# Performance work log

Measured on AMD Instinct MI355X. Metric: run time of the kernel, lower is better.

Reference implementation:

```python
import jax, jax.numpy as jnp
import numpy as np

N = 32768   # total nodes
E = 524288  # total edges (avg degree 16)
D = 128     # dim_h == input_size
H = 4       # attention heads
B = 64      # graphs per batch
S = 512     # nodes per graph (N = B*S, equal-size graphs)
EPS = 1e-5


def _lin(key, out_d, in_d):
    kw, kb = jax.random.split(key)
    s = 1.0 / np.sqrt(in_d)
    W = jax.random.uniform(kw, (out_d, in_d), minval=-s, maxval=s, dtype=jnp.float32)
    b = jax.random.uniform(kb, (out_d,), minval=-s, maxval=s, dtype=jnp.float32)
    return W, b


def setup_inputs() -> dict:
    key = jax.random.key(0)
    ks = jax.random.split(key, 16)
    x = jax.random.normal(ks[0], (N, D), dtype=jnp.float32)
    edge_index = jax.random.randint(ks[1], (2, E), 0, N, dtype=jnp.int64)
    batch_ids = (jnp.arange(N) // S).astype(jnp.int64)
    Wres, bres = _lin(ks[2], D, D)          # res_lin (MLPStack([in, dim_h]))
    Wk, bk = _lin(ks[3], D, D)              # ResGatedGraphConv lin_key
    Wq, bq = _lin(ks[4], D, D)              # lin_query
    Wv, bv = _lin(ks[5], D, D)              # lin_value
    Wskip, bskip = _lin(ks[6], D, D)        # lin_skip
    in_proj_w, in_proj_b = _lin(ks[7], 3 * D, D)   # MHA in_proj
    out_proj_w, out_proj_b = _lin(ks[8], D, D)     # MHA out_proj
    W1, b1 = _lin(ks[9], 2 * D, D)          # ff_linear1
    W2, b2 = _lin(ks[10], D, 2 * D)         # ff_linear2
    g1l = jax.random.normal(ks[11], (D,), dtype=jnp.float32) * 0.1 + 1.0
    b1l = jax.random.normal(ks[12], (D,), dtype=jnp.float32) * 0.1
    g1a = jax.random.normal(ks[13], (D,), dtype=jnp.float32) * 0.1 + 1.0
    b1a = jax.random.normal(ks[14], (D,), dtype=jnp.float32) * 0.1
    kg, kb2 = jax.random.split(ks[15])
    g2 = jax.random.normal(kg, (D,), dtype=jnp.float32) * 0.1 + 1.0
    b2g = jax.random.normal(kb2, (D,), dtype=jnp.float32) * 0.1
    return dict(x=x, edge_index=edge_index, batch_ids=batch_ids,
                Wres=Wres, bres=bres, Wk=Wk, bk=bk, Wq=Wq, bq=bq, Wv=Wv, bv=bv,
                Wskip=Wskip, bskip=bskip, g1l=g1l, b1l=b1l, g1a=g1a, b1a=b1a,
                in_proj_w=in_proj_w, in_proj_b=in_proj_b,
                out_proj_w=out_proj_w, out_proj_b=out_proj_b,
                W1=W1, b1=b1, W2=W2, b2=b2, g2=g2, b2g=b2g)


def _bn(h, g, b):
    # BatchNorm1d in eval mode, running_mean=0, running_var=1
    return h * (g / jnp.sqrt(1.0 + EPS)) + b


def _forward(x, edge_index, Wres, bres, Wk, bk, Wq, bq, Wv, bv, Wskip, bskip,
             g1l, b1l, g1a, b1a, in_proj_w, in_proj_b, out_proj_w, out_proj_b,
             W1, b1, W2, b2, g2, b2g):
    src, dst = edge_index[0], edge_index[1]
    # residual projection (MLPStack([input_size, dim_h]) -> Linear + ReLU)
    h_in1 = jax.nn.relu(x @ Wres.T + bres)

    # --- local: ResGatedGraphConv ---
    k = x @ Wk.T + bk   # keyed by target node
    q = x @ Wq.T + bq   # queried by source node
    v = x @ Wv.T + bv
    msg = jax.nn.sigmoid(k[dst] + q[src]) * v[src]                 # [E, D]
    agg = jax.ops.segment_sum(msg, dst, num_segments=N)            # [N, D]
    h_local = agg + (x @ Wskip.T + bskip)
    h_local = _bn(h_in1 + h_local, g1l, b1l)

    # --- global: dense-batch multihead attention (equal graphs, no padding) ---
    hd = D // H
    h_dense = h_in1.reshape(B, S, D)
    qkv = h_dense @ in_proj_w.T + in_proj_b                        # [B, S, 3D]
    qh, kh, vh = jnp.split(qkv, 3, axis=-1)
    qh = qh.reshape(B, S, H, hd)
    kh = kh.reshape(B, S, H, hd)
    vh = vh.reshape(B, S, H, hd)
    scores = jnp.einsum('bqhd,bkhd->bhqk', qh, kh) / np.sqrt(hd)   # [B, H, S, S]
    attn = jax.nn.softmax(scores, axis=-1)
    ctx = jnp.einsum('bhqk,bkhd->bqhd', attn, vh).reshape(B, S, D)
    h_attn = (ctx @ out_proj_w.T + out_proj_b).reshape(N, D)
    h_attn = _bn(h_in1 + h_attn, g1a, b1a)

    # --- combine + FFN ---
    h = h_local + h_attn
    ff = jax.nn.relu(h @ W1.T + b1) @ W2.T + b2
    h = _bn(h + ff, g2, b2g)
    return h


def reference(x, edge_index, batch_ids, Wres, bres, Wk, bk, Wq, bq, Wv, bv,
              Wskip, bskip, g1l, b1l, g1a, b1a, in_proj_w, in_proj_b,
              out_proj_w, out_proj_b, W1, b1, W2, b2, g2, b2g):
    return _forward(x, edge_index, Wres, bres, Wk, bk, Wq, bq, Wv, bv,
                    Wskip, bskip, g1l, b1l, g1a, b1a, in_proj_w, in_proj_b,
                    out_proj_w, out_proj_b, W1, b1, W2, b2, g2, b2g)
```

## Files before the change

### kernel.cpp

```cpp
#include <hip/hip_runtime.h>
#include <math.h>

#define N_NODES 32768
#define N_EDGES 524288
#define DIM     128
#define CAP     80

static constexpr size_t NM = (size_t)N_NODES * DIM;

typedef __attribute__((ext_vector_type(8)))  short bf8;
typedef __attribute__((ext_vector_type(4)))  float f32x4;
typedef __attribute__((ext_vector_type(16))) float f32x16;

__device__ __forceinline__ short f2bs(float x) {
    union { float f; unsigned int u; } v; v.f = x;
    unsigned int r = v.u + 0x7fffu + ((v.u >> 16) & 1u);
    return (short)(r >> 16);
}
__device__ __forceinline__ unsigned int pk2(float a, float b) {
    return (unsigned int)(unsigned short)f2bs(a) |
           ((unsigned int)(unsigned short)f2bs(b) << 16);
}
__device__ __forceinline__ float2 bs2f(unsigned int u) {
    union { unsigned int a; float f; } lo, hi;
    lo.a = u << 16; hi.a = u & 0xffff0000u;
    float2 r; r.x = lo.f; r.y = hi.f; return r;
}
__device__ __forceinline__ float bs1f(short s) {
    union { unsigned int a; float f; } t;
    t.a = ((unsigned int)(unsigned short)s) << 16; return t.f;
}

__global__ __launch_bounds__(256)
void cvt_scatter_kernel(const float* __restrict__ x,
                        const float* __restrict__ w0, const float* __restrict__ w1,
                        const float* __restrict__ w2, const float* __restrict__ w3,
                        const float* __restrict__ w4, const float* __restrict__ w5,
                        const float* __restrict__ w6, const float* __restrict__ w7,
                        const float* __restrict__ w8,
                        const float* __restrict__ b0, const float* __restrict__ b1,
                        const float* __restrict__ b2, const float* __restrict__ b3,
                        const float* __restrict__ b4,
                        const int* __restrict__ ei,
                        short* __restrict__ xb, short* __restrict__ wbf,
                        float* __restrict__ bcat,
                        int* __restrict__ deg, unsigned short* __restrict__ slots)
{
    if (blockIdx.x < 2048) {
        int e = blockIdx.x * 256 + threadIdx.x;
        int d = ei[N_EDGES + e];
        int pos = atomicAdd(&deg[d], 1);
        if (pos < CAP) slots[d * CAP + pos] = (unsigned short)ei[e];
        return;
    }
    long long t = (long long)(blockIdx.x - 2048) * 256 + threadIdx.x;
    long long i4 = t * 4;
    if (i4 < (long long)NM) {
        float4 v = *(const float4*)(x + i4);
        short4 o; o.x = f2bs(v.x); o.y = f2bs(v.y); o.z = f2bs(v.z); o.w = f2bs(v.w);
        *(short4*)(xb + i4) = o;
    } else {
        int j = (int)(i4 - (long long)NM);
        if (j < 212992) {
            const float* src; int off;
            if      (j <  16384) { src = w0; off = 0; }
            else if (j <  32768) { src = w1; off = 16384; }
            else if (j <  49152) { src = w2; off = 32768; }
            else if (j <  65536) { src = w3; off = 49152; }
            else if (j <  81920) { src = w4; off = 65536; }
            else if (j < 131072) { src = w5; off = 81920; }
            else if (j < 147456) { src = w6; off = 131072; }
            else if (j < 180224) { src = w7; off = 147456; }
            else                 { src = w8; off = 180224; }
            float4 v = *(const float4*)(src + (j - off));
            short4 o; o.x = f2bs(v.x); o.y = f2bs(v.y); o.z = f2bs(v.z); o.w = f2bs(v.w);
            *(short4*)(wbf + j) = o;
        } else if (j < 213632) {
            int jb = j - 212992;
            int grp = jb >> 7, loc = jb & 127;
            const float* bs = (grp == 0) ? b0 : (grp == 1) ? b1 :
                              (grp == 2) ? b2 : (grp == 3) ? b3 : b4;
            float4 v = *(const float4*)(bs + loc);
            *(float4*)(bcat + jb) = v;
        }
    }
}

__global__ __launch_bounds__(256)
void proj5_kernel(const short* __restrict__ xb, const short* __restrict__ wbf,
                  const float* __restrict__ bcat,
                  short* __restrict__ hin1b, short* __restrict__ kbv,
                  short* __restrict__ qvb, short* __restrict__ skipb)
{
    const int g  = blockIdx.x / 512;
    const int my = blockIdx.x % 512;
    const int lane = threadIdx.x & 63;
    const int wid  = threadIdx.x >> 6;
    const int m0 = my * 64 + (wid >> 1) * 32;
    const int n0 = (wid & 1) * 64;
    const int lrow = lane & 15;
    const int lk   = (lane >> 4) * 8;

    f32x4 acc[2][4] = {};
    const short* Ap = xb + (size_t)(m0 + lrow) * 128 + lk;
    const short* Wp = wbf + g * 16384 + (size_t)(n0 + lrow) * 128 + lk;
    #pragma unroll
    for (int ks = 0; ks < 128; ks += 32) {
        bf8 af[2], wf[4];
        af[0] = *(const bf8*)(Ap + ks);
        af[1] = *(const bf8*)(Ap + 16 * 128 + ks);
        #pragma unroll
        for (int j = 0; j < 4; ++j) wf[j] = *(const bf8*)(Wp + (size_t)j * 16 * 128 + ks);
        #pragma unroll
        for (int i = 0; i < 2; ++i)
            #pragma unroll
            for (int j = 0; j < 4; ++j)
                acc[i][j] = __builtin_amdgcn_mfma_f32_16x16x32_bf16(af[i], wf[j], acc[i][j], 0, 0, 0);
    }
    const int rbase = (lane >> 4) * 4;
    #pragma unroll
    for (int j = 0; j < 4; ++j) {
        int col = n0 + j * 16 + lrow;
        float bcol = bcat[g * 128 + col];
        #pragma unroll
        for (int i = 0; i < 2; ++i)
            #pragma unroll
            for (int r = 0; r < 4; ++r) {
                int row = m0 + i * 16 + rbase + r;
                float v = acc[i][j][r] + bcol;
                if (g == 0)      { v = fmaxf(v, 0.f); hin1b[(size_t)row * 128 + col] = f2bs(v); }
                else if (g == 1) kbv[(size_t)row * 128 + col] = f2bs(v);
                else if (g == 2) qvb[(size_t)row * 256 + col * 2] = f2bs(v);
                else if (g == 3) qvb[(size_t)row * 256 + col * 2 + 1] = f2bs(v);
                else             skipb[(size_t)row * 128 + col] = f2bs(v);
            }
    }
}

__global__ __launch_bounds__(256)
void inproj_kernel(const short* __restrict__ hin1b, const short* __restrict__ wbf,
                   const float* __restrict__ bin, short* __restrict__ qkvb,
                   float qscale)
{
    const int gx = blockIdx.x % 3;
    const int my = blockIdx.x / 3;
    const int lane = threadIdx.x & 63;
    const int wid  = threadIdx.x >> 6;
    const int m0 = my * 64 + (wid >> 1) * 32;
    const int n0 = (wid & 1) * 64;
    const int lrow = lane & 15;
    const int lk   = (lane >> 4) * 8;

    f32x4 acc[2][4] = {};
    const short* Ap = hin1b + (size_t)(m0 + lrow) * 128 + lk;
    const short* Wp = wbf + 81920 + (size_t)(gx * 128 + n0 + lrow) * 128 + lk;
    #pragma unroll
    for (int ks = 0; ks < 128; ks += 32) {
        bf8 af[2], wf[4];
        af[0] = *(const bf8*)(Ap + ks);
        af[1] = *(const bf8*)(Ap + 16 * 128 + ks);
        #pragma unroll
        for (int j = 0; j < 4; ++j) wf[j] = *(const bf8*)(Wp + (size_t)j * 16 * 128 + ks);
        #pragma unroll
        for (int i = 0; i < 2; ++i)
            #pragma unroll
            for (int j = 0; j < 4; ++j)
                acc[i][j] = __builtin_amdgcn_mfma_f32_16x16x32_bf16(af[i], wf[j], acc[i][j], 0, 0, 0);
    }
    const int rbase = (lane >> 4) * 4;
    #pragma unroll
    for (int j = 0; j < 4; ++j) {
        int col = gx * 128 + n0 + j * 16 + lrow;
        float bcol = bin[col];
        float sc = (col < 128) ? qscale : 1.0f;
        #pragma unroll
        for (int i = 0; i < 2; ++i)
            #pragma unroll
            for (int r = 0; r < 4; ++r) {
                int row = m0 + i * 16 + rbase + r;
                float v = (acc[i][j][r] + bcol) * sc;
                qkvb[(size_t)row * 384 + col] = f2bs(v);
            }
    }
}

__global__ __launch_bounds__(256)
void gather_local_kernel(const unsigned int* __restrict__ kbu,
                         const uint2* __restrict__ qvu,
                         const unsigned int* __restrict__ skipu,
                         const unsigned int* __restrict__ hin1u,
                         const int* __restrict__ deg,
                         const unsigned short* __restrict__ slots,
                         const float* __restrict__ g, const float* __restrict__ beta,
                         unsigned int* __restrict__ hlocal_u)
{
    const int d    = blockIdx.x * 4 + (threadIdx.x >> 6);
    const int lane = threadIdx.x & 63;
    const float rs = 0.9999950000374998f;

    float2 k2 = bs2f(kbu[(size_t)d * 64 + lane]);
    int dg = deg[d]; if (dg > CAP) dg = CAP;
    const unsigned short* sp = slots + (size_t)d * CAP;
    int i = 0;

    float ax = 0.f, ay = 0.f, cx = 0.f, cy = 0.f;
    for (; i + 8 <= dg; i += 8) {
        int s[8];
        #pragma unroll
        for (int u = 0; u < 8; ++u) s[u] = sp[i + u];
        uint2 w[8];
        #pragma unroll
        for (int u = 0; u < 8; ++u) w[u] = qvu[(size_t)s[u] * 64 + lane];
        #pragma unroll
        for (int u = 0; u < 8; ++u) {
            float2 pa = bs2f(w[u].x), pb = bs2f(w[u].y);
            if (u & 1) {
                cx += pa.y * __builtin_amdgcn_rcpf(1.0f + __expf(-(k2.x + pa.x)));
                cy += pb.y * __builtin_amdgcn_rcpf(1.0f + __expf(-(k2.y + pb.x)));
            } else {
                ax += pa.y * __builtin_amdgcn_rcpf(1.0f + __expf(-(k2.x + pa.x)));
                ay += pb.y * __builtin_amdgcn_rcpf(1.0f + __expf(-(k2.y + pb.x)));
            }
        }
    }
    for (; i + 4 <= dg; i += 4) {
        int s0 = sp[i], s1 = sp[i + 1], s2 = sp[i + 2], s3 = sp[i + 3];
        uint2 w0 = qvu[(size_t)s0 * 64 + lane];
        uint2 w1 = qvu[(size_t)s1 * 64 + lane];
        uint2 w2 = qvu[(size_t)s2 * 64 + lane];
        uint2 w3 = qvu[(size_t)s3 * 64 + lane];
        float2 p0 = bs2f(w0.x), p1 = bs2f(w0.y);
        float2 p2 = bs2f(w1.x), p3 = bs2f(w1.y);
        float2 p4 = bs2f(w2.x), p5 = bs2f(w2.y);
        float2 p6 = bs2f(w3.x), p7 = bs2f(w3.y);
        ax += p0.y * __builtin_amdgcn_rcpf(1.0f + __expf(-(k2.x + p0.x)));
        ay += p1.y * __builtin_amdgcn_rcpf(1.0f + __expf(-(k2.y + p1.x)));
        cx += p2.y * __builtin_amdgcn_rcpf(1.0f + __expf(-(k2.x + p2.x)));
        cy += p3.y * __builtin_amdgcn_rcpf(1.0f + __expf(-(k2.y + p3.x)));
        ax += p4.y * __builtin_amdgcn_rcpf(1.0f + __expf(-(k2.x + p4.x)));
        ay += p5.y * __builtin_amdgcn_rcpf(1.0f + __expf(-(k2.y + p5.x)));
        cx += p6.y * __builtin_amdgcn_rcpf(1.0f + __expf(-(k2.x + p6.x)));
        cy += p7.y * __builtin_amdgcn_rcpf(1.0f + __expf(-(k2.y + p7.x)));
    }
    for (; i < dg; ++i) {
        int s0 = sp[i];
        uint2 w0 = qvu[(size_t)s0 * 64 + lane];
        float2 p0 = bs2f(w0.x), p1 = bs2f(w0.y);
        ax += p0.y * __builtin_amdgcn_rcpf(1.0f + __expf(-(k2.x + p0.x)));
        ay += p1.y * __builtin_amdgcn_rcpf(1.0f + __expf(-(k2.y + p1.x)));
    }
    ax += cx; ay += cy;

    float2 sk = bs2f(skipu[(size_t)d * 64 + lane]);
    float2 hi = bs2f(hin1u[(size_t)d * 64 + lane]);
    float2 gv = *(const float2*)(g + lane * 2);
    float2 bt = *(const float2*)(beta + lane * 2);
    float ox = (hi.x + sk.x + ax) * (gv.x * rs) + bt.x;
    float oy = (hi.y + sk.y + ay) * (gv.y * rs) + bt.y;
    hlocal_u[(size_t)d * 64 + lane] = pk2(ox, oy);
}

__device__ __forceinline__ void lswap(unsigned int& X, unsigned int& Y, bool hi) {
    unsigned int Xs = (unsigned int)__shfl_xor((int)X, 32);
    unsigned int Ys = (unsigned int)__shfl_xor((int)Y, 32);
    unsigned int Xn = hi ? Ys : X;
    unsigned int Yn = hi ? Y  : Xs;
    X = Xn; Y = Yn;
}

__global__ __launch_bounds__(512)
void attn_mfma(const short* __restrict__ qkv, short* __restrict__ ctx)
{
    __shared__ __align__(16) char lds[36864];

    const int blk  = blockIdx.x;
    const int h    = blk & 3;
    const int b    = blk >> 2;
    const int tid  = threadIdx.x;
    const int lane = tid & 63;
    const int wid  = tid >> 6;
    const int lq = lane & 31;
    const int lg = lane >> 5;
    const size_t gbase = (size_t)(b * 512) * 384 + h * 32;

    const int skey  = tid >> 2;
    const int spart = tid & 3;
    const int vp    = tid & 63;
    const int vdq   = tid >> 6;

    bf8    kst;
    short4 v0s, v1s;

    #define STAGE_LOAD(ck)                                                     \
        kst = *(const bf8*)(qkv + gbase +                                      \
                (size_t)((ck) * 128 + skey) * 384 + 128 + spart * 8);          \
        {                                                                      \
            const short* vr = qkv + gbase +                                    \
                (size_t)((ck) * 128 + 2 * vp) * 384 + 256 + vdq * 4;           \
            v0s = *(const short4*)(vr);                                        \
            v1s = *(const short4*)(vr + 384);                                  \
        }

    #define STAGE_WRITE(s)                                                     \
        *(bf8*)((short*)(lds + (s) * 10240) + skey * 40 + spart * 8) = kst;    \
        {                                                                      \
            char* vb = lds + 20480 + (s) * 8192;                               \
            short v0a[4] = {v0s.x, v0s.y, v0s.z, v0s.w};                       \
            short v1a[4] = {v1s.x, v1s.y, v1s.z, v1s.w};                       \
            _Pragma("unroll")                                                  \
            for (int j = 0; j < 4; ++j) {                                      \
                int d = vdq * 4 + j;                                           \
                unsigned int w = (unsigned int)(unsigned short)v0a[j] |        \
                                 ((unsigned int)(unsigned short)v1a[j] << 16); \
                *(unsigned int*)(vb + d * 256 + ((4 * vp) ^ ((d & 7) << 4))) = w; \
            }                                                                  \
        }

    const int qoff = wid * 64;
    bf8 qf[2][2];
    #pragma unroll
    for (int qg = 0; qg < 2; ++qg)
        #pragma unroll
        for (int kh = 0; kh < 2; ++kh)
            qf[qg][kh] = *(const bf8*)(qkv + gbase +
                           (size_t)(qoff + qg * 32 + lq) * 384 + kh * 16 + lg * 8);

    const f32x16 Z16 = {0.f,0.f,0.f,0.f,0.f,0.f,0.f,0.f,0.f,0.f,0.f,0.f,0.f,0.f,0.f,0.f};
    f32x16 o[2] = {Z16, Z16};
    float mreg[2] = {-1e30f, -1e30f};
    float lreg[2] = {0.f, 0.f};
    const bool hiw = (lg != 0);

    STAGE_LOAD(0);
    STAGE_WRITE(0);
    __syncthreads();

    for (int c = 0; c < 4; ++c) {
        if (c < 3) { STAGE_LOAD(c + 1); }
        const short* Kb = (const short*)(lds + (c & 1) * 10240);
        const char*  Vb = lds + 20480 + (c & 1) * 8192;

        #pragma unroll
        for (int ktl = 0; ktl < 4; ++ktl) {
            bf8 ak[2], vt[2];
            #pragma unroll
            for (int kh = 0; kh < 2; ++kh) {
                ak[kh] = *(const bf8*)(Kb + (ktl * 32 + lq) * 40 + kh * 16 + lg * 8);
                int kbyte = (ktl * 32 + kh * 16 + lg * 8) * 2;
                vt[kh] = *(const bf8*)(Vb + lq * 256 + (kbyte ^ ((lq & 7) << 4)));
            }
            #pragma unroll
            for (int qg = 0; qg < 2; ++qg) {
                f32x16 s = Z16;
                s = __builtin_amdgcn_mfma_f32_32x32x16_bf16(ak[0], qf[qg][0], s, 0, 0, 0);
                s = __builtin_amdgcn_mfma_f32_32x32x16_bf16(ak[1], qf[qg][1], s, 0, 0, 0);
                float t0 = fmaxf(fmaxf(s[0],  s[1]),  s[2]);
                float t1 = fmaxf(fmaxf(s[3],  s[4]),  s[5]);
                float t2 = fmaxf(fmaxf(s[6],  s[7]),  s[8]);
                float t3 = fmaxf(fmaxf(s[9],  s[10]), s[11]);
                float t4 = fmaxf(fmaxf(s[12], s[13]), s[14]);
                float mt = fmaxf(fmaxf(fmaxf(t0, t1), t2), fmaxf(fmaxf(t3, t4), s[15]));
                mt = fmaxf(mt, __shfl_xor(mt, 32));
                if (__any(mt > mreg[qg] + 11.5415603f)) {
                    float mnew = fmaxf(mreg[qg], mt);
                    float corr = exp2f(mreg[qg] - mnew);
                    mreg[qg] = mnew;
                    lreg[qg] *= corr;
                    #pragma unroll
                    for (int r = 0; r < 16; ++r) o[qg][r] *= corr;
                }
                float m = mreg[qg];
                float p[16]; float ps = 0.f;
                #pragma unroll
                for (int r = 0; r < 16; ++r) { p[r] = exp2f(s[r] - m); ps += p[r]; }
                ps += __shfl_xor(ps, 32);
                lreg[qg] += ps;
                unsigned int w0 = pk2(p[0],  p[1]),  w1 = pk2(p[2],  p[3]);
                unsigned int w2 = pk2(p[4],  p[5]),  w3 = pk2(p[6],  p[7]);
                unsigned int w4 = pk2(p[8],  p[9]),  w5 = pk2(p[10], p[11]);
                unsigned int w6 = pk2(p[12], p[13]), w7 = pk2(p[14], p[15]);
                lswap(w0, w2, hiw); lswap(w1, w3, hiw);
                lswap(w4, w6, hiw); lswap(w5, w7, hiw);
                union { unsigned int u[4]; bf8 v; } P0, P1;
                P0.u[0] = w0; P0.u[1] = w1; P0.u[2] = w2; P0.u[3] = w3;
                P1.u[0] = w4; P1.u[1] = w5; P1.u[2] = w6; P1.u[3] = w7;
                o[qg] = __builtin_amdgcn_mfma_f32_32x32x16_bf16(vt[0], P0.v, o[qg], 0, 0, 0);
                o[qg] = __builtin_amdgcn_mfma_f32_32x32x16_bf16(vt[1], P1.v, o[qg], 0, 0, 0);
            }
        }
        if (c < 3) { STAGE_WRITE((c + 1) & 1); }
        __syncthreads();
    }
    #undef STAGE_LOAD
    #undef STAGE_WRITE

    #pragma unroll
    for (int qg = 0; qg < 2; ++qg) {
        float inv = 1.0f / lreg[qg];
        int ql = qoff + qg * 32 + lq;
        #pragma unroll
        for (int b4 = 0; b4 < 4; ++b4) {
            short4 pkv;
            pkv.x = f2bs(o[qg][b4 * 4 + 0] * inv);
            pkv.y = f2bs(o[qg][b4 * 4 + 1] * inv);
            pkv.z = f2bs(o[qg][b4 * 4 + 2] * inv);
            pkv.w = f2bs(o[qg][b4 * 4 + 3] * inv);
            int dbyte = (8 * b4 + 4 * lg) * 2;
            *(short4*)(lds + ql * 64 + (dbyte ^ ((ql & 7) << 3))) = pkv;
        }
    }
    __syncthreads();
    {
        int ql = tid;
        short* dst = ctx + (size_t)(b * 512 + ql) * 128 + h * 32;
        #pragma unroll
        for (int i = 0; i < 8; ++i) {
            short4 part = *(short4*)(lds + ql * 64 + ((i * 8) ^ ((ql & 7) << 3)));
            *(short4*)(dst + i * 4) = part;
        }
    }
}

__global__ __launch_bounds__(256)
void outproj_ff_kernel(const short* __restrict__ ctxb, const short* __restrict__ wbf,
                       const float* __restrict__ bout,
                       const short* __restrict__ hin1b, const short* __restrict__ hlocb,
                       const float* __restrict__ g1a, const float* __restrict__ b1a,
                       const float* __restrict__ b1, const float* __restrict__ b2,
                       const float* __restrict__ g2, const float* __restrict__ b2g,
                       float* __restrict__ out)
{
    __shared__ __align__(16) short ldsH[64 * 128];
    __shared__ __align__(16) short ldsF[64 * 256];
    const int my = blockIdx.x;
    const int lane = threadIdx.x & 63;
    const int wid  = threadIdx.x >> 6;
    const int lrow = lane & 15;
    const int lk   = (lane >> 4) * 8;
    const int rbase = (lane >> 4) * 4;
    const float rs = 0.9999950000374998f;

    {
        const int m0 = (wid >> 1) * 32;
        const int n0 = (wid & 1) * 64;
        f32x4 acc[2][4] = {};
        const short* Ap = ctxb + (size_t)(my * 64 + m0 + lrow) * 128 + lk;
        const short* Wp = wbf + 131072 + (size_t)(n0 + lrow) * 128 + lk;
        #pragma unroll
        for (int ks = 0; ks < 128; ks += 32) {
            bf8 af[2], wf[4];
            af[0] = *(const bf8*)(Ap + ks);
            af[1] = *(const bf8*)(Ap + 16 * 128 + ks);
            #pragma unroll
            for (int j = 0; j < 4; ++j) wf[j] = *(const bf8*)(Wp + (size_t)j * 16 * 128 + ks);
            #pragma unroll
            for (int i = 0; i < 2; ++i)
                #pragma unroll
                for (int j = 0; j < 4; ++j)
                    acc[i][j] = __builtin_amdgcn_mfma_f32_16x16x32_bf16(af[i], wf[j], acc[i][j], 0, 0, 0);
        }
        #pragma unroll
        for (int j = 0; j < 4; ++j) {
            int col = n0 + j * 16 + lrow;
            float bcol = bout[col];
            float gsc = g1a[col] * rs;
            float bsc = b1a[col];
            #pragma unroll
            for (int i = 0; i < 2; ++i)
                #pragma unroll
                for (int r = 0; r < 4; ++r) {
                    int rl = m0 + i * 16 + rbase + r;
                    size_t idx = (size_t)(my * 64 + rl) * 128 + col;
                    float v = acc[i][j][r] + bcol;
                    float o = bs1f(hlocb[idx]) + (bs1f(hin1b[idx]) + v) * gsc + bsc;
                    int byte = (rl * 256 + col * 2) ^ ((rl & 7) << 4);
                    *(short*)((char*)ldsH + byte) = f2bs(o);
                }
        }
    }
    __syncthreads();
    {
        const int m0 = (wid >> 1) * 32;
        const int n0 = (wid & 1) * 128;
        f32x4 acc[2][8] = {};
        const short* Wp = wbf + 147456 + (size_t)(n0 + lrow) * 128 + lk;
        #pragma unroll
        for (int ks = 0; ks < 128; ks += 32) {
            bf8 af[2], wf[8];
            #pragma unroll
            for (int i = 0; i < 2; ++i) {
                int row = m0 + lrow + i * 16;
                int byte = (row * 256 + (ks + lk) * 2) ^ ((row & 7) << 4);
                af[i] = *(const bf8*)((const char*)ldsH + byte);
            }
            #pragma unroll
            for (int j = 0; j < 8; ++j) wf[j] = *(const bf8*)(Wp + (size_t)j * 16 * 128 + ks);
            #pragma unroll
            for (int i = 0; i < 2; ++i)
                #pragma unroll
                for (int j = 0; j < 8; ++j)
                    acc[i][j] = __builtin_amdgcn_mfma_f32_16x16x32_bf16(af[i], wf[j], acc[i][j], 0, 0, 0);
        }
        #pragma unroll
        for (int j = 0; j < 8; ++j) {
            int col = n0 + j * 16 + lrow;
            float bc = b1[col];
            #pragma unroll
            for (int i = 0; i < 2; ++i)
                #pragma unroll
                for (int r = 0; r < 4; ++r) {
                    int rl = m0 + i * 16 + rbase + r;
                    float v = fmaxf(acc[i][j][r] + bc, 0.f);
                    int byte = (rl * 512 + col * 2) ^ ((rl & 7) << 4);
                    *(short*)((char*)ldsF + byte) = f2bs(v);
                }
        }
    }
    __syncthreads();
    {
        const int m0 = (wid >> 1) * 32;
        const int n0 = (wid & 1) * 64;
        f32x4 acc[2][4] = {};
        const short* Wp = wbf + 180224 + (size_t)(n0 + lrow) * 256 + lk;
        #pragma unroll
        for (int ks = 0; ks < 256; ks += 32) {
            bf8 af[2], wf[4];
            #pragma unroll
            for (int i = 0; i < 2; ++i) {
                int row = m0 + lrow + i * 16;
                int byte = (row * 512 + (ks + lk) * 2) ^ ((row & 7) << 4);
                af[i] = *(const bf8*)((const char*)ldsF + byte);
            }
            #pragma unroll
            for (int j = 0; j < 4; ++j) wf[j] = *(const bf8*)(Wp + (size_t)j * 16 * 256 + ks);
            #pragma unroll
            for (int i = 0; i < 2; ++i)
                #pragma unroll
                for (int j = 0; j < 4; ++j)
                    acc[i][j] = __builtin_amdgcn_mfma_f32_16x16x32_bf16(af[i], wf[j], acc[i][j], 0, 0, 0);
        }
        #pragma unroll
        for (int j = 0; j < 4; ++j) {
            int col = n0 + j * 16 + lrow;
            float bc = b2[col];
            float gsc = g2[col] * rs;
            float bsc = b2g[col];
            #pragma unroll
            for (int i = 0; i < 2; ++i)
                #pragma unroll
                for (int r = 0; r < 4; ++r) {
                    int rl = m0 + i * 16 + rbase + r;
                    int hbyte = (rl * 256 + col * 2) ^ ((rl & 7) << 4);
                    float hres = bs1f(*(const short*)((const char*)ldsH + hbyte));
                    float v = acc[i][j][r] + bc;
                    out[(size_t)(my * 64 + rl) * 128 + col] = (hres + v) * gsc + bsc;
                }
        }
    }
}

extern "C" void kernel_launch(void* const* d_in, const int* in_sizes, int n_in,
                              void* d_out, int out_size, void* d_ws, size_t ws_size,
                              hipStream_t stream)
{
    (void)in_sizes; (void)n_in; (void)out_size; (void)ws_size;

    const float* x    = (const float*)d_in[0];
    const int*   ei   = (const int*)d_in[1];
    const float* Wres = (const float*)d_in[3];
    const float* bres = (const float*)d_in[4];
    const float* Wk   = (const float*)d_in[5];
    const float* bk   = (const float*)d_in[6];
    const float* Wq   = (const float*)d_in[7];
    const float* bq   = (const float*)d_in[8];
    const float* Wv   = (const float*)d_in[9];
    const float* bv   = (const float*)d_in[10];
    const float* Wsk  = (const float*)d_in[11];
    const float* bsk  = (const float*)d_in[12];
    const float* g1l  = (const float*)d_in[13];
    const float* b1l  = (const float*)d_in[14];
    const float* g1a  = (const float*)d_in[15];
    const float* b1a  = (const float*)d_in[16];
    const float* Win  = (const float*)d_in[17];
    const float* bin  = (const float*)d_in[18];
    const float* Wout = (const float*)d_in[19];
    const float* bout = (const float*)d_in[20];
    const float* W1   = (const float*)d_in[21];
    const float* b1   = (const float*)d_in[22];
    const float* W2   = (const float*)d_in[23];
    const float* b2   = (const float*)d_in[24];
    const float* g2   = (const float*)d_in[25];
    const float* b2g  = (const float*)d_in[26];
    float* out = (float*)d_out;

    float* ws = (float*)d_ws;
    short* hin1b = (short*)ws;
    short* kbv   = (short*)(ws + NM / 2);
    short* qvb   = (short*)(ws + NM);
    short* skipb = (short*)(ws + 2 * NM);
    short* xb    = (short*)(ws + 2 * NM + NM / 2);
    short* qkvb  = (short*)(ws + 3 * NM);
    short* hlocb = (short*)(ws + 4 * NM + NM / 2);
    int* deg = (int*)(ws + 5 * NM);
    unsigned short* slots = (unsigned short*)(deg + N_NODES);
    short* ctxb  = (short*)(ws + 5 * NM);
    short* wbf   = (short*)(ws + 6 * NM);
    float* bcat  = ws + 6 * NM + 106496;

    dim3 blk(256);
    const float qscale = 0.17677669529663687f * 1.4426950408889634f;

    hipMemsetAsync((void*)deg, 0, N_NODES * sizeof(int), stream);

    cvt_scatter_kernel<<<dim3(6353), blk, 0, stream>>>(
        x, Wres, Wk, Wq, Wv, Wsk, Win, Wout, W1, W2,
        bres, bk, bq, bv, bsk, ei, xb, wbf, bcat, deg, slots);

    proj5_kernel<<<dim3(2560), blk, 0, stream>>>(
        xb, wbf, bcat, hin1b, kbv, qvb, skipb);

    inproj_kernel<<<dim3(1536), blk, 0, stream>>>(
        hin1b, wbf, bin, qkvb, qscale);

    gather_local_kernel<<<dim3(N_NODES / 4), blk, 0, stream>>>(
        (const unsigned int*)kbv, (const uint2*)qvb, (const unsigned int*)skipb,
        (const unsigned int*)hin1b, deg, slots, g1l, b1l,
        (unsigned int*)hlocb);

    attn_mfma<<<dim3(256), dim3(512), 0, stream>>>(qkvb, ctxb);

    outproj_ff_kernel<<<dim3(512), blk, 0, stream>>>(
        ctxb, wbf, bout, hin1b, hlocb, g1a, b1a, b1, b2, g2, b2g, out);
}
```

Measured before the change: 205.7 us.

## Split attention query rows across two blocks per head and truncate P to bf16

The attention kernel now launches twice as many blocks. Each block covers half of a graph's queries for one head, and each wave handles 32 query rows instead of 64. On a chip with 256 CUs, 256 blocks means about one block per CU, so this raises occupancy and cuts per-thread register pressure. The cost is that K/V staging is repeated in both blocks. The softmax probabilities are also packed to bf16 by truncation instead of round-to-nearest, which saves ALU work but adds a small bias.

```diff
diff --git a/kernel.cpp b/kernel.cpp
--- a/kernel.cpp
+++ b/kernel.cpp
@@ -20,6 +20,10 @@
 __device__ __forceinline__ unsigned int pk2(float a, float b) {
     return (unsigned int)(unsigned short)f2bs(a) |
            ((unsigned int)(unsigned short)f2bs(b) << 16);
+}
+__device__ __forceinline__ unsigned int pk2t(float a, float b) {
+    union { float f; unsigned int u; } ua, ub; ua.f = a; ub.f = b;
+    return (ua.u >> 16) | (ub.u & 0xffff0000u);
 }
 __device__ __forceinline__ float2 bs2f(unsigned int u) {
     union { unsigned int a; float f; } lo, hi;
@@ -274,8 +278,9 @@
     __shared__ __align__(16) char lds[36864];
 
     const int blk  = blockIdx.x;
-    const int h    = blk & 3;
-    const int b    = blk >> 2;
+    const int half = blk & 1;
+    const int h    = (blk >> 1) & 3;
+    const int b    = blk >> 3;
     const int tid  = threadIdx.x;
     const int lane = tid & 63;
     const int wid  = tid >> 6;
@@ -316,19 +321,17 @@
             }                                                                  \
         }
 
-    const int qoff = wid * 64;
-    bf8 qf[2][2];
+    const int qoff = half * 256 + wid * 32;
+    bf8 qf[2];
     #pragma unroll
-    for (int qg = 0; qg < 2; ++qg)
-        #pragma unroll
-        for (int kh = 0; kh < 2; ++kh)
-            qf[qg][kh] = *(const bf8*)(qkv + gbase +
-                           (size_t)(qoff + qg * 32 + lq) * 384 + kh * 16 + lg * 8);
+    for (int kh = 0; kh < 2; ++kh)
+        qf[kh] = *(const bf8*)(qkv + gbase +
+                       (size_t)(qoff + lq) * 384 + kh * 16 + lg * 8);
 
     const f32x16 Z16 = {0.f,0.f,0.f,0.f,0.f,0.f,0.f,0.f,0.f,0.f,0.f,0.f,0.f,0.f,0.f,0.f};
-    f32x16 o[2] = {Z16, Z16};
-    float mreg[2] = {-1e30f, -1e30f};
-    float lreg[2] = {0.f, 0.f};
+    f32x16 o = Z16;
+    float mreg = -1e30f;
+    float lreg = 0.f;
     const bool hiw = (lg != 0);
 
     STAGE_LOAD(0);
@@ -349,44 +352,41 @@
                 int kbyte = (ktl * 32 + kh * 16 + lg * 8) * 2;
                 vt[kh] = *(const bf8*)(Vb + lq * 256 + (kbyte ^ ((lq & 7) << 4)));
             }
-            #pragma unroll
-            for (int qg = 0; qg < 2; ++qg) {
-                f32x16 s = Z16;
-                s = __builtin_amdgcn_mfma_f32_32x32x16_bf16(ak[0], qf[qg][0], s, 0, 0, 0);
-                s = __builtin_amdgcn_mfma_f32_32x32x16_bf16(ak[1], qf[qg][1], s, 0, 0, 0);
-                float t0 = fmaxf(fmaxf(s[0],  s[1]),  s[2]);
-                float t1 = fmaxf(fmaxf(s[3],  s[4]),  s[5]);
-                float t2 = fmaxf(fmaxf(s[6],  s[7]),  s[8]);
-                float t3 = fmaxf(fmaxf(s[9],  s[10]), s[11]);
-                float t4 = fmaxf(fmaxf(s[12], s[13]), s[14]);
-                float mt = fmaxf(fmaxf(fmaxf(t0, t1), t2), fmaxf(fmaxf(t3, t4), s[15]));
-                mt = fmaxf(mt, __shfl_xor(mt, 32));
-                if (__any(mt > mreg[qg] + 11.5415603f)) {
-                    float mnew = fmaxf(mreg[qg], mt);
-                    float corr = exp2f(mreg[qg] - mnew);
-                    mreg[qg] = mnew;
-                    lreg[qg] *= corr;
-                    #pragma unroll
-                    for (int r = 0; r < 16; ++r) o[qg][r] *= corr;
-                }
-                float m = mreg[qg];
-                float p[16]; float ps = 0.f;
+            f32x16 s = Z16;
+            s = __builtin_amdgcn_mfma_f32_32x32x16_bf16(ak[0], qf[0], s, 0, 0, 0);
+            s = __builtin_amdgcn_mfma_f32_32x32x16_bf16(ak[1], qf[1], s, 0, 0, 0);
+            float t0 = fmaxf(fmaxf(s[0],  s[1]),  s[2]);
+            float t1 = fmaxf(fmaxf(s[3],  s[4]),  s[5]);
+            float t2 = fmaxf(fmaxf(s[6],  s[7]),  s[8]);
+            float t3 = fmaxf(fmaxf(s[9],  s[10]), s[11]);
+            float t4 = fmaxf(fmaxf(s[12], s[13]), s[14]);
+            float mt = fmaxf(fmaxf(fmaxf(t0, t1), t2), fmaxf(fmaxf(t3, t4), s[15]));
+            mt = fmaxf(mt, __shfl_xor(mt, 32));
+            if (__any(mt > mreg + 11.5415603f)) {
+                float mnew = fmaxf(mreg, mt);
+                float corr = exp2f(mreg - mnew);
+                mreg = mnew;
+                lreg *= corr;
                 #pragma unroll
-                for (int r = 0; r < 16; ++r) { p[r] = exp2f(s[r] - m); ps += p[r]; }
-                ps += __shfl_xor(ps, 32);
-                lreg[qg] += ps;
-                unsigned int w0 = pk2(p[0],  p[1]),  w1 = pk2(p[2],  p[3]);
-                unsigned int w2 = pk2(p[4],  p[5]),  w3 = pk2(p[6],  p[7]);
-                unsigned int w4 = pk2(p[8],  p[9]),  w5 = pk2(p[10], p[11]);
-                unsigned int w6 = pk2(p[12], p[13]), w7 = pk2(p[14], p[15]);
-                lswap(w0, w2, hiw); lswap(w1, w3, hiw);
-                lswap(w4, w6, hiw); lswap(w5, w7, hiw);
-                union { unsigned int u[4]; bf8 v; } P0, P1;
-                P0.u[0] = w0; P0.u[1] = w1; P0.u[2] = w2; P0.u[3] = w3;
-                P1.u[0] = w4; P1.u[1] = w5; P1.u[2] = w6; P1.u[3] = w7;
-                o[qg] = __builtin_amdgcn_mfma_f32_32x32x16_bf16(vt[0], P0.v, o[qg], 0, 0, 0);
-                o[qg] = __builtin_amdgcn_mfma_f32_32x32x16_bf16(vt[1], P1.v, o[qg], 0, 0, 0);
+                for (int r = 0; r < 16; ++r) o[r] *= corr;
             }
+            float m = mreg;
+            float p[16]; float ps = 0.f;
+            #pragma unroll
+            for (int r = 0; r < 16; ++r) { p[r] = exp2f(s[r] - m); ps += p[r]; }
+            ps += __shfl_xor(ps, 32);
+            lreg += ps;
+            unsigned int w0 = pk2t(p[0],  p[1]),  w1 = pk2t(p[2],  p[3]);
+            unsigned int w2 = pk2t(p[4],  p[5]),  w3 = pk2t(p[6],  p[7]);
+            unsigned int w4 = pk2t(p[8],  p[9]),  w5 = pk2t(p[10], p[11]);
+            unsigned int w6 = pk2t(p[12], p[13]), w7 = pk2t(p[14], p[15]);
+            lswap(w0, w2, hiw); lswap(w1, w3, hiw);
+            lswap(w4, w6, hiw); lswap(w5, w7, hiw);
+            union { unsigned int u[4]; bf8 v; } P0, P1;
+            P0.u[0] = w0; P0.u[1] = w1; P0.u[2] = w2; P0.u[3] = w3;
+            P1.u[0] = w4; P1.u[1] = w5; P1.u[2] = w6; P1.u[3] = w7;
+            o = __builtin_amdgcn_mfma_f32_32x32x16_bf16(vt[0], P0.v, o, 0, 0, 0);
+            o = __builtin_amdgcn_mfma_f32_32x32x16_bf16(vt[1], P1.v, o, 0, 0, 0);
         }
         if (c < 3) { STAGE_WRITE((c + 1) & 1); }
         __syncthreads();
@@ -394,29 +394,30 @@
     #undef STAGE_LOAD
     #undef STAGE_WRITE
 
-    #pragma unroll
-    for (int qg = 0; qg < 2; ++qg) {
-        float inv = 1.0f / lreg[qg];
-        int ql = qoff + qg * 32 + lq;
+    {
+        float inv = 1.0f / lreg;
+        int ql = wid * 32 + lq;
         #pragma unroll
         for (int b4 = 0; b4 < 4; ++b4) {
             short4 pkv;
-            pkv.x = f2bs(o[qg][b4 * 4 + 0] * inv);
-            pkv.y = f2bs(o[qg][b4 * 4 + 1] * inv);
-            pkv.z = f2bs(o[qg][b4 * 4 + 2] * inv);
-            pkv.w = f2bs(o[qg][b4 * 4 + 3] * inv);
+            pkv.x = f2bs(o[b4 * 4 + 0] * inv);
+            pkv.y = f2bs(o[b4 * 4 + 1] * inv);
+            pkv.z = f2bs(o[b4 * 4 + 2] * inv);
+            pkv.w = f2bs(o[b4 * 4 + 3] * inv);
             int dbyte = (8 * b4 + 4 * lg) * 2;
             *(short4*)(lds + ql * 64 + (dbyte ^ ((ql & 7) << 3))) = pkv;
         }
     }
     __syncthreads();
     {
-        int ql = tid;
-        short* dst = ctx + (size_t)(b * 512 + ql) * 128 + h * 32;
-        #pragma unroll
-        for (int i = 0; i < 8; ++i) {
-            short4 part = *(short4*)(lds + ql * 64 + ((i * 8) ^ ((ql & 7) << 3)));
-            *(short4*)(dst + i * 4) = part;
+        int row  = tid >> 1;
+        int pbase = (tid & 1) * 4;
+        short* dst = ctx + (size_t)(b * 512 + half * 256 + row) * 128 + h * 32;
+        #pragma unroll
+        for (int i = 0; i < 4; ++i) {
+            int part = pbase + i;
+            short4 pv = *(short4*)(lds + row * 64 + ((part * 8) ^ ((row & 7) << 3)));
+            *(short4*)(dst + part * 4) = pv;
         }
     }
 }
@@ -627,7 +628,7 @@
         (const unsigned int*)hin1b, deg, slots, g1l, b1l,
         (unsigned int*)hlocb);
 
-    attn_mfma<<<dim3(256), dim3(512), 0, stream>>>(qkvb, ctxb);
+    attn_mfma<<<dim3(512), dim3(512), 0, stream>>>(qkvb, ctxb);
 
     outproj_ff_kernel<<<dim3(512), blk, 0, stream>>>(
         ctxb, wbf, bout, hin1b, hlocb, g1a, b1a, b1, b2, g2, b2g, out);
```

After: 195.5 us. 5.0% less time.
